# Performance work log

Measured on AMD Instinct MI355X. Metric: run time of the kernel, lower is better.

## Reference

```python
import jax, jax.numpy as jnp
import numpy as np
from jax import lax

INT8_NARROW = (-127.0, 127.0)   # brevitas Int8WeightPerTensorFloat (narrow range)
INT8_FULL = (-128.0, 127.0)     # brevitas Int8ActPerTensorFloat
INT32 = (-2.0**31, 2.0**31 - 1)


def _fake_quant(v, scale, qmin, qmax):
    # round-to-nearest, clip, dequant (per-tensor)
    return jnp.clip(jnp.round(v / scale), qmin, qmax) * scale


def _conv(x, w, stride):
    return lax.conv_general_dilated(
        x, w, window_strides=(stride, stride), padding=[(1, 1), (1, 1)],
        dimension_numbers=("NCHW", "OIHW", "NCHW"))


def setup_inputs() -> dict:
    key = jax.random.key(0)
    ks = jax.random.split(key, 5)
    B, Cin, Cout, H = 64, 256, 512, 28
    x = jax.random.normal(ks[0], (B, Cin, H, H), dtype=jnp.float32)
    w1 = jax.random.normal(ks[1], (Cout, Cin, 3, 3), dtype=jnp.float32) * 0.05
    b1 = jax.random.normal(ks[2], (Cout,), dtype=jnp.float32) * 0.01
    w2 = jax.random.normal(ks[3], (Cout, Cout, 3, 3), dtype=jnp.float32) * 0.05
    b2 = jax.random.normal(ks[4], (Cout,), dtype=jnp.float32) * 0.01
    return {
        "x": x, "w1": w1, "b1": b1, "w2": w2, "b2": b2,
        "in_scale": jnp.full((1,), 0.05, dtype=jnp.float32),
        "act1_scale": jnp.full((1,), 0.05, dtype=jnp.float32),
        "act2_scale": jnp.full((1,), 0.05, dtype=jnp.float32),
    }


def reference(x, w1, b1, w2, b2, in_scale, act1_scale, act2_scale):
    s_in = in_scale[0]
    s_a1 = act1_scale[0]
    s_a2 = act2_scale[0]

    # conv1: per-tensor int8 weight fake-quant (max-abs stats, narrow range)
    s_w1 = jnp.max(jnp.abs(w1)) / 127.0
    wq1 = _fake_quant(w1, s_w1, *INT8_NARROW)
    bq1 = _fake_quant(b1, s_in * s_w1, *INT32)  # Int32Bias: scale = in_scale*w_scale
    out = _conv(x, wq1, 2) + bq1[None, :, None, None]

    # act1: int8 activation fake-quant (learned per-tensor scale)
    out = _fake_quant(out, s_a1, *INT8_FULL)

    # conv2
    s_w2 = jnp.max(jnp.abs(w2)) / 127.0
    wq2 = _fake_quant(w2, s_w2, *INT8_NARROW)
    bq2 = _fake_quant(b2, s_a1 * s_w2, *INT32)
    out = _conv(out, wq2, 1) + bq2[None, :, None, None]

    # act2
    out = _fake_quant(out, s_a2, *INT8_FULL)
    return out
```

## Files before the change

kernel.cpp:

```cpp
#include <hip/hip_runtime.h>

typedef int i32x4 __attribute__((ext_vector_type(4)));

__device__ __forceinline__ void gl_lds16(const signed char* g, signed char* l) {
    __builtin_amdgcn_global_load_lds(
        (const __attribute__((address_space(1))) void*)g,
        (__attribute__((address_space(3))) void*)l, 16, 0, 0);
}

__device__ __forceinline__ unsigned lds_addr(const signed char* p) {
    return (unsigned)(uintptr_t)(const __attribute__((address_space(3))) signed char*)p;
}

__device__ __forceinline__ i32x4 lds_read_b128a(unsigned a) {
    i32x4 r;
    asm volatile("ds_read_b128 %0, %1" : "=v"(r) : "v"(a));
    return r;
}

#define XQ_SCALE 2048.0f
#define XQ_DELTA (1.0f / 2048.0f)

__device__ __forceinline__ float block_max256(const float* __restrict__ part, int base,
                                              float* __restrict__ sred) {
    float m = part[base + (threadIdx.x & 255)];
#pragma unroll
    for (int off = 32; off > 0; off >>= 1)
        m = fmaxf(m, __shfl_down(m, off));
    __syncthreads();
    if ((threadIdx.x & 63) == 0) sred[threadIdx.x >> 6] = m;
    __syncthreads();
    return fmaxf(fmaxf(sred[0], sred[1]), fmaxf(sred[2], sred[3]));
}

__global__ __launch_bounds__(256) void fused_pre_kernel(
    const float* __restrict__ x,
    const float* __restrict__ w1, const float* __restrict__ w2,
    float* __restrict__ part,
    signed char* __restrict__ xhi, signed char* __restrict__ xlo,
    signed char* __restrict__ act) {
    __shared__ float sred[4];
    const int blk = blockIdx.x;
    const int tid = threadIdx.x;
    const uint4 z = {0, 0, 0, 0};

    if (blk < 512) {
        const bool second = blk >= 256;
        const float* w = second ? w2 : w1;
        const int n4 = second ? 589824 : 294912;
        float m = 0.0f;
        for (int i = (blk & 255) * 256 + tid; i < n4; i += 65536) {
            float4 v = ((const float4*)w)[i];
            m = fmaxf(m, fmaxf(fmaxf(fabsf(v.x), fabsf(v.y)), fmaxf(fabsf(v.z), fabsf(v.w))));
        }
#pragma unroll
        for (int off = 32; off > 0; off >>= 1)
            m = fmaxf(m, __shfl_down(m, off));
        if ((tid & 63) == 0) sred[tid >> 6] = m;
        __syncthreads();
        if (tid == 0)
            part[blk] = fmaxf(fmaxf(sred[0], sred[1]), fmaxf(sred[2], sred[3]));
    } else if (blk < 976) {
        const int thr = (blk - 512) * 256 + tid;
        const int b = thr / (116 * 16);
        const int rr = thr - b * (116 * 16);
        const int p = rr >> 4;
        const int ch = rr & 15;
        int h, w;
        if (p < 30)      { h = 0;          w = p; }
        else if (p < 60) { h = 29;         w = p - 30; }
        else if (p < 88) { h = p - 60 + 1; w = 0; }
        else             { h = p - 88 + 1; w = 29; }
        const int off = (b * 900 + h * 30 + w) * 256 + ch * 16;
        *(uint4*)(xhi + off) = z;
        *(uint4*)(xlo + off) = z;
    } else if (blk < 1456) {
        const int thr = (blk - 976) * 256 + tid;
        const int b = thr / (60 * 32);
        const int rr = thr - b * (60 * 32);
        const int p = rr >> 5;
        const int ch = rr & 31;
        int h, w;
        if (p < 16)      { h = 0;          w = p; }
        else if (p < 32) { h = 15;         w = p - 16; }
        else if (p < 46) { h = p - 32 + 1; w = 0; }
        else             { h = p - 46 + 1; w = 15; }
        const int off = (b * 256 + h * 16 + w) * 512 + ch * 16;
        *(uint4*)(act + off) = z;
    } else {
        const int xb = blk - 1456;
        const int hwb = xb % 25;
        const int rest = xb / 25;
        const int cb = rest & 1;
        const int b = rest >> 1;
        const int c0 = cb * 128 + (tid >> 5) * 16;
        const int hw = hwb * 32 + (tid & 31);
        if (hw < 784) {
            const float* xp = x + (b * 256 + c0) * 784 + hw;
            union { signed char c[16]; uint4 u; } ph, pl;
#pragma unroll
            for (int j = 0; j < 16; ++j) {
                const float v = xp[j * 784];
                int q = (int)rintf(v * XQ_SCALE);
                q = max(-16383, min(16383, q));
                ph.c[j] = (signed char)(q >> 7);
                pl.c[j] = (signed char)(q & 127);
            }
            const int r = hw / 28;
            const int o = (b * 900 + (r + 1) * 30 + (hw - r * 28) + 1) * 256 + c0;
            *(uint4*)&xhi[o] = ph.u;
            *(uint4*)&xlo[o] = pl.u;
        }
    }
}

__global__ __launch_bounds__(256) void prep_w_kernel(
    const float* __restrict__ w1, const float* __restrict__ w2,
    const float* __restrict__ b1, const float* __restrict__ b2,
    const float* __restrict__ part,
    const float* __restrict__ in_scale, const float* __restrict__ act1_scale,
    signed char* __restrict__ wq1, signed char* __restrict__ wq2,
    float* __restrict__ bq1, float* __restrict__ bq2,
    float* __restrict__ wmax) {
    __shared__ __align__(16) signed char sw[4608];
    __shared__ float sred[4];
    const int blk = blockIdx.x;
    const int tid = threadIdx.x;

    if (blk < 512) {
        const float inv_s = 127.0f / block_max256(part, 0, sred);
        const int n = blk;
        const float4* src = (const float4*)(w1 + n * 2304);
#pragma unroll
        for (int rd = 0; rd < 3; ++rd) {
            const int f = rd * 256 + tid;
            if (f < 576) {
                const float4 v = src[f];
                float q0 = fminf(fmaxf(rintf(v.x * inv_s), -127.0f), 127.0f);
                float q1 = fminf(fmaxf(rintf(v.y * inv_s), -127.0f), 127.0f);
                float q2 = fminf(fmaxf(rintf(v.z * inv_s), -127.0f), 127.0f);
                float q3 = fminf(fmaxf(rintf(v.w * inv_s), -127.0f), 127.0f);
                const int i0 = f * 4;
                int cin, r;
                cin = i0 / 9;       r = i0 - cin * 9;       sw[r * 256 + cin] = (signed char)(int)q0;
                cin = (i0+1) / 9;   r = (i0+1) - cin * 9;   sw[r * 256 + cin] = (signed char)(int)q1;
                cin = (i0+2) / 9;   r = (i0+2) - cin * 9;   sw[r * 256 + cin] = (signed char)(int)q2;
                cin = (i0+3) / 9;   r = (i0+3) - cin * 9;   sw[r * 256 + cin] = (signed char)(int)q3;
            }
        }
        __syncthreads();
        if (tid < 144) *(uint4*)&wq1[n * 2304 + tid * 16] = *(const uint4*)&sw[tid * 16];
    } else if (blk < 1024) {
        const float inv_s = 127.0f / block_max256(part, 256, sred);
        const int n = blk - 512;
        const float4* src = (const float4*)(w2 + n * 4608);
#pragma unroll
        for (int rd = 0; rd < 5; ++rd) {
            const int f = rd * 256 + tid;
            if (f < 1152) {
                const float4 v = src[f];
                float q0 = fminf(fmaxf(rintf(v.x * inv_s), -127.0f), 127.0f);
                float q1 = fminf(fmaxf(rintf(v.y * inv_s), -127.0f), 127.0f);
                float q2 = fminf(fmaxf(rintf(v.z * inv_s), -127.0f), 127.0f);
                float q3 = fminf(fmaxf(rintf(v.w * inv_s), -127.0f), 127.0f);
                const int i0 = f * 4;
                int cin, r;
                cin = i0 / 9;       r = i0 - cin * 9;       sw[r * 512 + cin] = (signed char)(int)q0;
                cin = (i0+1) / 9;   r = (i0+1) - cin * 9;   sw[r * 512 + cin] = (signed char)(int)q1;
                cin = (i0+2) / 9;   r = (i0+2) - cin * 9;   sw[r * 512 + cin] = (signed char)(int)q2;
                cin = (i0+3) / 9;   r = (i0+3) - cin * 9;   sw[r * 512 + cin] = (signed char)(int)q3;
            }
        }
        __syncthreads();
        for (int o = tid; o < 288; o += 256)
            *(uint4*)&wq2[n * 4608 + o * 16] = *(const uint4*)&sw[o * 16];
    } else {
        const float m1 = block_max256(part, 0, sred);
        const float m2 = block_max256(part, 256, sred);
        if (tid == 0) { wmax[0] = m1; wmax[1] = m2; }
        for (int idx = tid; idx < 1024; idx += 256) {
            if (idx < 512) {
                const float s = (*in_scale) * (m1 * (1.0f / 127.0f));
                float q = rintf(b1[idx] / s);
                q = fminf(fmaxf(q, -2147483648.0f), 2147483648.0f);
                bq1[idx] = q * s;
            } else {
                const int j = idx - 512;
                const float s = (*act1_scale) * (m2 * (1.0f / 127.0f));
                float q = rintf(b2[j] / s);
                q = fminf(fmaxf(q, -2147483648.0f), 2147483648.0f);
                bq2[j] = q * s;
            }
        }
    }
}

template<int CIN, int STRIDE, int HP, int HOUT, bool SPLIT, bool FINAL>
__global__ __launch_bounds__(256, SPLIT ? 2 : 3) void conv_gemm_kernel(
    const signed char* __restrict__ Ahi,
    const signed char* __restrict__ Alo,
    const signed char* __restrict__ Wt,
    const float* __restrict__ bias,
    const float* __restrict__ wmax,
    const float* __restrict__ s_pre,
    const float* __restrict__ s_act,
    signed char* __restrict__ act_out,
    float* __restrict__ out_final)
{
    constexpr int K = 9 * CIN;
    constexpr int HW = HOUT * HOUT;
    constexpr int NIT = K / 128;
    constexpr int NC = SPLIT ? 8 : 6;
    constexpr int BUFSZ = SPLIT ? 32768 : 24576;
    constexpr int NB = SPLIT ? 4 : 2;

    __shared__ __align__(16) signed char smem[2 * BUFSZ];

    const int tid = threadIdx.x;
    const int lane = tid & 63;
    const int wv = tid >> 6;
    const int pair = wv >> 1;
    const int nh = wv & 1;
    const int quad = lane >> 4;
    const int l16 = lane & 15;

    const int lin = blockIdx.x + (int)gridDim.x * blockIdx.y;
    const int swz = (lin & 7) * 98 + (lin >> 3);
    const int n0 = (swz & 3) * 128;
    const int m0 = (swz >> 2) * 64;

    const int lrow = lane >> 3;
    const int koff = ((lane & 7) ^ lrow) * 16;

    const signed char* srcb[NC];
    int dsto[NC];
    bool isA[NC];
    if constexpr (SPLIT) {
#pragma unroll
        for (int i = 0; i < NC; ++i) {
            const int g = wv * 8 + i;
            const int type = g >> 3;
            if (type >= 2) {
                const int c = g - 16;
                srcb[i] = Wt + (n0 + c * 8 + lrow) * K + koff;
                dsto[i] = 16384 + c * 1024;
                isA[i] = false;
            } else {
                const int c = g & 7;
                const int m = m0 + c * 8 + lrow;
                const int b = m / HW;
                const int rem = m - b * HW;
                const int oh = rem / HOUT;
                const int ow = rem - oh * HOUT;
                const int off = ((b * HP + oh * STRIDE) * HP + ow * STRIDE) * CIN + koff;
                srcb[i] = (type == 0 ? Ahi : Alo) + off;
                dsto[i] = type * 8192 + c * 1024;
                isA[i] = true;
            }
        }
    } else {
#pragma unroll
        for (int i = 0; i < NC; ++i) {
            const int g = wv * 6 + i;
            if (g < 8) {
                const int c = g;
                const int m = m0 + c * 8 + lrow;
                const int b = m / HW;
                const int rem = m - b * HW;
                const int oh = rem / HOUT;
                const int ow = rem - oh * HOUT;
                const int off = ((b * HP + oh * STRIDE) * HP + ow * STRIDE) * CIN + koff;
                srcb[i] = Ahi + off;
                dsto[i] = c * 1024;
                isA[i] = true;
            } else {
                const int c = g - 8;
                srcb[i] = Wt + (n0 + c * 8 + lrow) * K + koff;
                dsto[i] = 8192 + c * 1024;
                isA[i] = false;
            }
        }
    }

    const int aoff0 = SPLIT ? (pair * 8192) : 0;
    const int boff0 = SPLIT ? 16384 : 8192;
    const int nfix  = SPLIT ? (nh * 64) : (wv * 32);

    unsigned aad[2][2][4];
    unsigned bad[2][2][NB];
#pragma unroll
    for (int bi = 0; bi < 2; ++bi)
#pragma unroll
        for (int ks = 0; ks < 2; ++ks) {
#pragma unroll
            for (int mi = 0; mi < 4; ++mi) {
                const int row = mi * 16 + l16;
                const int sl = ((ks * 4 + quad) ^ (row & 7)) * 16;
                aad[bi][ks][mi] = lds_addr(&smem[bi * BUFSZ + aoff0 + row * 128 + sl]);
            }
#pragma unroll
            for (int ni = 0; ni < NB; ++ni) {
                const int row = nfix + ni * 16 + l16;
                const int sl = ((ks * 4 + quad) ^ (row & 7)) * 16;
                bad[bi][ks][ni] = lds_addr(&smem[bi * BUFSZ + boff0 + row * 128 + sl]);
            }
        }

    i32x4 acc[4][NB];
#pragma unroll
    for (int mi = 0; mi < 4; ++mi)
#pragma unroll
        for (int ni = 0; ni < NB; ++ni)
            acc[mi][ni] = i32x4{0, 0, 0, 0};

    auto STAGE = [&](int bo, int it) {
        const int k0 = it * 128;
        const int r9 = k0 / CIN;
        const int kh = r9 / 3;
        const int kw = r9 - kh * 3;
        const int ashift = (kh * HP + kw) * CIN + (k0 & (CIN - 1));
#pragma unroll
        for (int i = 0; i < NC; ++i)
            gl_lds16(srcb[i] + (isA[i] ? ashift : k0), &smem[bo + dsto[i]]);
    };

    i32x4 af[2][4], bf[2][NB];

    auto LOADFRAGS = [&](int bi) {
#pragma unroll
        for (int ks = 0; ks < 2; ++ks) {
#pragma unroll
            for (int mi = 0; mi < 4; ++mi)
                af[ks][mi] = lds_read_b128a(aad[bi][ks][mi]);
#pragma unroll
            for (int ni = 0; ni < NB; ++ni)
                bf[ks][ni] = lds_read_b128a(bad[bi][ks][ni]);
        }
    };

    auto MFMAS_KS = [&](int ks) {
        __builtin_amdgcn_s_setprio(1);
#pragma unroll
        for (int mi = 0; mi < 4; ++mi)
#pragma unroll
            for (int ni = 0; ni < NB; ++ni)
                acc[mi][ni] = __builtin_amdgcn_mfma_i32_16x16x64_i8(af[ks][mi], bf[ks][ni], acc[mi][ni], 0, 0, 0);
        __builtin_amdgcn_s_setprio(0);
    };

    auto WAIT_NC = [&]() {
        if constexpr (SPLIT) asm volatile("s_waitcnt vmcnt(8)" ::: "memory");
        else                 asm volatile("s_waitcnt vmcnt(6)" ::: "memory");
    };
    auto LGKM_HALF = [&]() {
        if constexpr (SPLIT) asm volatile("s_waitcnt lgkmcnt(8)" ::: "memory");
        else                 asm volatile("s_waitcnt lgkmcnt(6)" ::: "memory");
    };

    STAGE(0, 0);
    STAGE(BUFSZ, 1);

    for (int it = 0; it < NIT - 2; it += 2) {
        WAIT_NC();
        __builtin_amdgcn_s_barrier();
        __builtin_amdgcn_sched_barrier(0);
        LOADFRAGS(0);
        LGKM_HALF();
        __builtin_amdgcn_sched_barrier(0);
        MFMAS_KS(0);
        asm volatile("s_waitcnt lgkmcnt(0)" ::: "memory");
        __builtin_amdgcn_sched_barrier(0);
        __builtin_amdgcn_s_barrier();
        __builtin_amdgcn_sched_barrier(0);
        STAGE(0, it + 2);
        MFMAS_KS(1);

        WAIT_NC();
        __builtin_amdgcn_s_barrier();
        __builtin_amdgcn_sched_barrier(0);
        LOADFRAGS(1);
        LGKM_HALF();
        __builtin_amdgcn_sched_barrier(0);
        MFMAS_KS(0);
        asm volatile("s_waitcnt lgkmcnt(0)" ::: "memory");
        __builtin_amdgcn_sched_barrier(0);
        __builtin_amdgcn_s_barrier();
        __builtin_amdgcn_sched_barrier(0);
        if (it + 3 < NIT) STAGE(BUFSZ, it + 3);
        MFMAS_KS(1);
    }

    WAIT_NC();
    __builtin_amdgcn_s_barrier();
    __builtin_amdgcn_sched_barrier(0);
    LOADFRAGS(0);
    LGKM_HALF();
    __builtin_amdgcn_sched_barrier(0);
    MFMAS_KS(0);
    asm volatile("s_waitcnt lgkmcnt(0)" ::: "memory");
    __builtin_amdgcn_sched_barrier(0);
    MFMAS_KS(1);

    asm volatile("s_waitcnt vmcnt(0)" ::: "memory");
    __builtin_amdgcn_s_barrier();
    __builtin_amdgcn_sched_barrier(0);
    LOADFRAGS(1);
    LGKM_HALF();
    __builtin_amdgcn_sched_barrier(0);
    MFMAS_KS(0);
    asm volatile("s_waitcnt lgkmcnt(0)" ::: "memory");
    __builtin_amdgcn_sched_barrier(0);
    MFMAS_KS(1);

    if constexpr (SPLIT) {
        __syncthreads();
        if (pair == 1) {
#pragma unroll
            for (int mi = 0; mi < 4; ++mi)
#pragma unroll
                for (int ni = 0; ni < 4; ++ni)
                    *(i32x4*)&smem[nh * 16384 + (mi * 4 + ni) * 1024 + lane * 16] = acc[mi][ni];
        }
        __syncthreads();
        if (pair == 1) return;
#pragma unroll
        for (int mi = 0; mi < 4; ++mi)
#pragma unroll
            for (int ni = 0; ni < 4; ++ni) {
                const i32x4 other = *(const i32x4*)&smem[nh * 16384 + (mi * 4 + ni) * 1024 + lane * 16];
                acc[mi][ni] = acc[mi][ni] * 128 + other;
            }
    }

    float alpha = (*wmax) * (1.0f / 127.0f);
    if (FINAL) alpha *= *s_pre;
    if (SPLIT) alpha *= XQ_DELTA;
    const float sact = *s_act;

    float bv[NB];
#pragma unroll
    for (int ni = 0; ni < NB; ++ni)
        bv[ni] = bias[n0 + nfix + ni * 16 + l16];

#pragma unroll
    for (int mi = 0; mi < 4; ++mi) {
#pragma unroll
        for (int i = 0; i < 4; ++i) {
            const int m = m0 + mi * 16 + quad * 4 + i;
            const int b = m / HW;
            const int rem = m - b * HW;
            const int oh = rem / HOUT;
            const int ow = rem - oh * HOUT;
#pragma unroll
            for (int ni = 0; ni < NB; ++ni) {
                const int col = n0 + nfix + ni * 16 + l16;
                const float v = (float)acc[mi][ni][i] * alpha + bv[ni];
                float q = rintf(v / sact);
                q = fminf(fmaxf(q, -128.0f), 127.0f);
                if (FINAL) {
                    out_final[(b * 512 + col) * HW + oh * HOUT + ow] = q * sact;
                } else {
                    act_out[(b * 256 + (oh + 1) * 16 + (ow + 1)) * 512 + col] = (signed char)(int)q;
                }
            }
        }
    }
}

extern "C" void kernel_launch(void* const* d_in, const int* in_sizes, int n_in,
                              void* d_out, int out_size, void* d_ws, size_t ws_size,
                              hipStream_t stream) {
    const float* x  = (const float*)d_in[0];
    const float* w1 = (const float*)d_in[1];
    const float* b1 = (const float*)d_in[2];
    const float* w2 = (const float*)d_in[3];
    const float* b2 = (const float*)d_in[4];
    const float* in_scale   = (const float*)d_in[5];
    const float* act1_scale = (const float*)d_in[6];
    const float* act2_scale = (const float*)d_in[7];
    float* out = (float*)d_out;

    char* ws = (char*)d_ws;
    float* part = (float*)(ws + 0);
    float* wmax = (float*)(ws + 2048);
    float* bq1 = (float*)(ws + 2176);
    float* bq2 = (float*)(ws + 4224);
    signed char* wq1 = (signed char*)(ws + 8192);
    signed char* wq2 = (signed char*)(ws + 1187840);
    signed char* xhi = (signed char*)(ws + 3547136);
    signed char* xlo = (signed char*)(ws + 18292736);
    signed char* act = (signed char*)(ws + 33038336);

    fused_pre_kernel<<<4656, 256, 0, stream>>>(x, w1, w2, part, xhi, xlo, act);

    prep_w_kernel<<<1025, 256, 0, stream>>>(w1, w2, b1, b2, part, in_scale, act1_scale,
                                            wq1, wq2, bq1, bq2, wmax);

    conv_gemm_kernel<256, 2, 30, 14, true, false><<<dim3(4, 196), 256, 0, stream>>>(
        xhi, xlo, wq1, bq1, wmax, act1_scale, act1_scale, act, nullptr);

    conv_gemm_kernel<512, 1, 16, 14, false, true><<<dim3(4, 196), 256, 0, stream>>>(
        act, nullptr, wq2, bq2, wmax + 1, act1_scale, act2_scale, nullptr, out);
}
```

Baseline: 221.3 us.

## Merge weight max-reduction and quantization into one kernel with grid-wide atomic barrier

Folds the per-tensor weight abs-max reduction and the weight/bias quantization into a single pre-processing kernel. Each of the first 1024 blocks reduces its own output channel, publishes the result via atomicMax plus a counter, then spin-waits until all 512 blocks of that tensor arrive before quantizing. A memset clears the counters. This removes one kernel launch and re-reads the weights while they are likely still cached, but relies on all 1024 spinning blocks being co-resident (launch bounds 8 per CU) to avoid deadlock, and adds spin-wait latency.

Result: slower. 346.3 us (+56.5%).

```diff
diff --git a/kernel.cpp b/kernel.cpp
--- a/kernel.cpp
+++ b/kernel.cpp
@@ -21,36 +21,33 @@
 #define XQ_SCALE 2048.0f
 #define XQ_DELTA (1.0f / 2048.0f)
 
-__device__ __forceinline__ float block_max256(const float* __restrict__ part, int base,
-                                              float* __restrict__ sred) {
-    float m = part[base + (threadIdx.x & 255)];
-#pragma unroll
-    for (int off = 32; off > 0; off >>= 1)
-        m = fmaxf(m, __shfl_down(m, off));
-    __syncthreads();
-    if ((threadIdx.x & 63) == 0) sred[threadIdx.x >> 6] = m;
-    __syncthreads();
-    return fmaxf(fmaxf(sred[0], sred[1]), fmaxf(sred[2], sred[3]));
-}
-
-__global__ __launch_bounds__(256) void fused_pre_kernel(
+__global__ __launch_bounds__(256, 8) void mega_pre_kernel(
     const float* __restrict__ x,
     const float* __restrict__ w1, const float* __restrict__ w2,
-    float* __restrict__ part,
+    const float* __restrict__ b1, const float* __restrict__ b2,
+    const float* __restrict__ in_scale, const float* __restrict__ act1_scale,
+    unsigned* __restrict__ syn,
+    float* __restrict__ wmax,
+    float* __restrict__ bq1, float* __restrict__ bq2,
+    signed char* __restrict__ wq1, signed char* __restrict__ wq2,
     signed char* __restrict__ xhi, signed char* __restrict__ xlo,
-    signed char* __restrict__ act) {
-    __shared__ float sred[4];
+    signed char* __restrict__ act)
+{
+    __shared__ __align__(16) signed char sw[4608];
+    __shared__ float sred[8];
     const int blk = blockIdx.x;
     const int tid = threadIdx.x;
     const uint4 z = {0, 0, 0, 0};
 
-    if (blk < 512) {
-        const bool second = blk >= 256;
-        const float* w = second ? w2 : w1;
-        const int n4 = second ? 589824 : 294912;
+    if (blk < 1024) {
+        const bool second = blk >= 512;
+        const int n = second ? (blk - 512) : blk;
+        const int NF = second ? 1152 : 576;
+        const float4* src = (const float4*)((second ? w2 : w1) + n * (NF * 4));
+
         float m = 0.0f;
-        for (int i = (blk & 255) * 256 + tid; i < n4; i += 65536) {
-            float4 v = ((const float4*)w)[i];
+        for (int f = tid; f < NF; f += 256) {
+            const float4 v = src[f];
             m = fmaxf(m, fmaxf(fmaxf(fabsf(v.x), fabsf(v.y)), fmaxf(fabsf(v.z), fabsf(v.w))));
         }
 #pragma unroll
@@ -58,10 +55,92 @@
             m = fmaxf(m, __shfl_down(m, off));
         if ((tid & 63) == 0) sred[tid >> 6] = m;
         __syncthreads();
-        if (tid == 0)
-            part[blk] = fmaxf(fmaxf(sred[0], sred[1]), fmaxf(sred[2], sred[3]));
-    } else if (blk < 976) {
-        const int thr = (blk - 512) * 256 + tid;
+        if (tid == 0) {
+            m = fmaxf(fmaxf(sred[0], sred[1]), fmaxf(sred[2], sred[3]));
+            const int ci = second ? 1 : 0;
+            atomicMax(&syn[2 + ci], __float_as_uint(m));
+            __hip_atomic_fetch_add(&syn[ci], 1u, __ATOMIC_RELEASE, __HIP_MEMORY_SCOPE_AGENT);
+            while (__hip_atomic_load(&syn[ci], __ATOMIC_ACQUIRE, __HIP_MEMORY_SCOPE_AGENT) < 512u)
+                __builtin_amdgcn_s_sleep(8);
+            sred[4] = __uint_as_float(
+                __hip_atomic_load(&syn[2 + ci], __ATOMIC_ACQUIRE, __HIP_MEMORY_SCOPE_AGENT));
+        }
+        __syncthreads();
+        const float inv_s = 127.0f / sred[4];
+
+        if (!second) {
+#pragma unroll
+            for (int rd = 0; rd < 3; ++rd) {
+                const int f = rd * 256 + tid;
+                if (f < 576) {
+                    const float4 v = src[f];
+                    float q0 = fminf(fmaxf(rintf(v.x * inv_s), -127.0f), 127.0f);
+                    float q1 = fminf(fmaxf(rintf(v.y * inv_s), -127.0f), 127.0f);
+                    float q2 = fminf(fmaxf(rintf(v.z * inv_s), -127.0f), 127.0f);
+                    float q3 = fminf(fmaxf(rintf(v.w * inv_s), -127.0f), 127.0f);
+                    const int i0 = f * 4;
+                    int cin, r;
+                    cin = i0 / 9;     r = i0 - cin * 9;     sw[r * 256 + cin] = (signed char)(int)q0;
+                    cin = (i0+1) / 9; r = (i0+1) - cin * 9; sw[r * 256 + cin] = (signed char)(int)q1;
+                    cin = (i0+2) / 9; r = (i0+2) - cin * 9; sw[r * 256 + cin] = (signed char)(int)q2;
+                    cin = (i0+3) / 9; r = (i0+3) - cin * 9; sw[r * 256 + cin] = (signed char)(int)q3;
+                }
+            }
+            __syncthreads();
+            if (tid < 144) *(uint4*)&wq1[n * 2304 + tid * 16] = *(const uint4*)&sw[tid * 16];
+        } else {
+#pragma unroll
+            for (int rd = 0; rd < 5; ++rd) {
+                const int f = rd * 256 + tid;
+                if (f < 1152) {
+                    const float4 v = src[f];
+                    float q0 = fminf(fmaxf(rintf(v.x * inv_s), -127.0f), 127.0f);
+                    float q1 = fminf(fmaxf(rintf(v.y * inv_s), -127.0f), 127.0f);
+                    float q2 = fminf(fmaxf(rintf(v.z * inv_s), -127.0f), 127.0f);
+                    float q3 = fminf(fmaxf(rintf(v.w * inv_s), -127.0f), 127.0f);
+                    const int i0 = f * 4;
+                    int cin, r;
+                    cin = i0 / 9;     r = i0 - cin * 9;     sw[r * 512 + cin] = (signed char)(int)q0;
+                    cin = (i0+1) / 9; r = (i0+1) - cin * 9; sw[r * 512 + cin] = (signed char)(int)q1;
+                    cin = (i0+2) / 9; r = (i0+2) - cin * 9; sw[r * 512 + cin] = (signed char)(int)q2;
+                    cin = (i0+3) / 9; r = (i0+3) - cin * 9; sw[r * 512 + cin] = (signed char)(int)q3;
+                }
+            }
+            __syncthreads();
+            for (int o = tid; o < 288; o += 256)
+                *(uint4*)&wq2[n * 4608 + o * 16] = *(const uint4*)&sw[o * 16];
+        }
+    } else if (blk == 1024) {
+        if (tid == 0) {
+            while (__hip_atomic_load(&syn[0], __ATOMIC_ACQUIRE, __HIP_MEMORY_SCOPE_AGENT) < 512u ||
+                   __hip_atomic_load(&syn[1], __ATOMIC_ACQUIRE, __HIP_MEMORY_SCOPE_AGENT) < 512u)
+                __builtin_amdgcn_s_sleep(8);
+            sred[4] = __uint_as_float(
+                __hip_atomic_load(&syn[2], __ATOMIC_ACQUIRE, __HIP_MEMORY_SCOPE_AGENT));
+            sred[5] = __uint_as_float(
+                __hip_atomic_load(&syn[3], __ATOMIC_ACQUIRE, __HIP_MEMORY_SCOPE_AGENT));
+            wmax[0] = sred[4];
+            wmax[1] = sred[5];
+        }
+        __syncthreads();
+        const float m1 = sred[4];
+        const float m2 = sred[5];
+        for (int idx = tid; idx < 1024; idx += 256) {
+            if (idx < 512) {
+                const float s = (*in_scale) * (m1 * (1.0f / 127.0f));
+                float q = rintf(b1[idx] / s);
+                q = fminf(fmaxf(q, -2147483648.0f), 2147483648.0f);
+                bq1[idx] = q * s;
+            } else {
+                const int j = idx - 512;
+                const float s = (*act1_scale) * (m2 * (1.0f / 127.0f));
+                float q = rintf(b2[j] / s);
+                q = fminf(fmaxf(q, -2147483648.0f), 2147483648.0f);
+                bq2[j] = q * s;
+            }
+        }
+    } else if (blk < 1489) {
+        const int thr = (blk - 1025) * 256 + tid;
         const int b = thr / (116 * 16);
         const int rr = thr - b * (116 * 16);
         const int p = rr >> 4;
@@ -74,8 +153,8 @@
         const int off = (b * 900 + h * 30 + w) * 256 + ch * 16;
         *(uint4*)(xhi + off) = z;
         *(uint4*)(xlo + off) = z;
-    } else if (blk < 1456) {
-        const int thr = (blk - 976) * 256 + tid;
+    } else if (blk < 1969) {
+        const int thr = (blk - 1489) * 256 + tid;
         const int b = thr / (60 * 32);
         const int rr = thr - b * (60 * 32);
         const int p = rr >> 5;
@@ -88,7 +167,7 @@
         const int off = (b * 256 + h * 16 + w) * 512 + ch * 16;
         *(uint4*)(act + off) = z;
     } else {
-        const int xb = blk - 1456;
+        const int xb = blk - 1969;
         const int hwb = xb % 25;
         const int rest = xb / 25;
         const int cb = rest & 1;
@@ -110,87 +189,6 @@
             const int o = (b * 900 + (r + 1) * 30 + (hw - r * 28) + 1) * 256 + c0;
             *(uint4*)&xhi[o] = ph.u;
             *(uint4*)&xlo[o] = pl.u;
-        }
-    }
-}
-
-__global__ __launch_bounds__(256) void prep_w_kernel(
-    const float* __restrict__ w1, const float* __restrict__ w2,
-    const float* __restrict__ b1, const float* __restrict__ b2,
-    const float* __restrict__ part,
-    const float* __restrict__ in_scale, const float* __restrict__ act1_scale,
-    signed char* __restrict__ wq1, signed char* __restrict__ wq2,
-    float* __restrict__ bq1, float* __restrict__ bq2,
-    float* __restrict__ wmax) {
-    __shared__ __align__(16) signed char sw[4608];
-    __shared__ float sred[4];
-    const int blk = blockIdx.x;
-    const int tid = threadIdx.x;
-
-    if (blk < 512) {
-        const float inv_s = 127.0f / block_max256(part, 0, sred);
-        const int n = blk;
-        const float4* src = (const float4*)(w1 + n * 2304);
-#pragma unroll
-        for (int rd = 0; rd < 3; ++rd) {
-            const int f = rd * 256 + tid;
-            if (f < 576) {
-                const float4 v = src[f];
-                float q0 = fminf(fmaxf(rintf(v.x * inv_s), -127.0f), 127.0f);
-                float q1 = fminf(fmaxf(rintf(v.y * inv_s), -127.0f), 127.0f);
-                float q2 = fminf(fmaxf(rintf(v.z * inv_s), -127.0f), 127.0f);
-                float q3 = fminf(fmaxf(rintf(v.w * inv_s), -127.0f), 127.0f);
-                const int i0 = f * 4;
-                int cin, r;
-                cin = i0 / 9;       r = i0 - cin * 9;       sw[r * 256 + cin] = (signed char)(int)q0;
-                cin = (i0+1) / 9;   r = (i0+1) - cin * 9;   sw[r * 256 + cin] = (signed char)(int)q1;
-                cin = (i0+2) / 9;   r = (i0+2) - cin * 9;   sw[r * 256 + cin] = (signed char)(int)q2;
-                cin = (i0+3) / 9;   r = (i0+3) - cin * 9;   sw[r * 256 + cin] = (signed char)(int)q3;
-            }
-        }
-        __syncthreads();
-        if (tid < 144) *(uint4*)&wq1[n * 2304 + tid * 16] = *(const uint4*)&sw[tid * 16];
-    } else if (blk < 1024) {
-        const float inv_s = 127.0f / block_max256(part, 256, sred);
-        const int n = blk - 512;
-        const float4* src = (const float4*)(w2 + n * 4608);
-#pragma unroll
-        for (int rd = 0; rd < 5; ++rd) {
-            const int f = rd * 256 + tid;
-            if (f < 1152) {
-                const float4 v = src[f];
-                float q0 = fminf(fmaxf(rintf(v.x * inv_s), -127.0f), 127.0f);
-                float q1 = fminf(fmaxf(rintf(v.y * inv_s), -127.0f), 127.0f);
-                float q2 = fminf(fmaxf(rintf(v.z * inv_s), -127.0f), 127.0f);
-                float q3 = fminf(fmaxf(rintf(v.w * inv_s), -127.0f), 127.0f);
-                const int i0 = f * 4;
-                int cin, r;
-                cin = i0 / 9;       r = i0 - cin * 9;       sw[r * 512 + cin] = (signed char)(int)q0;
-                cin = (i0+1) / 9;   r = (i0+1) - cin * 9;   sw[r * 512 + cin] = (signed char)(int)q1;
-                cin = (i0+2) / 9;   r = (i0+2) - cin * 9;   sw[r * 512 + cin] = (signed char)(int)q2;
-                cin = (i0+3) / 9;   r = (i0+3) - cin * 9;   sw[r * 512 + cin] = (signed char)(int)q3;
-            }
-        }
-        __syncthreads();
-        for (int o = tid; o < 288; o += 256)
-            *(uint4*)&wq2[n * 4608 + o * 16] = *(const uint4*)&sw[o * 16];
-    } else {
-        const float m1 = block_max256(part, 0, sred);
-        const float m2 = block_max256(part, 256, sred);
-        if (tid == 0) { wmax[0] = m1; wmax[1] = m2; }
-        for (int idx = tid; idx < 1024; idx += 256) {
-            if (idx < 512) {
-                const float s = (*in_scale) * (m1 * (1.0f / 127.0f));
-                float q = rintf(b1[idx] / s);
-                q = fminf(fmaxf(q, -2147483648.0f), 2147483648.0f);
-                bq1[idx] = q * s;
-            } else {
-                const int j = idx - 512;
-                const float s = (*act1_scale) * (m2 * (1.0f / 127.0f));
-                float q = rintf(b2[j] / s);
-                q = fminf(fmaxf(q, -2147483648.0f), 2147483648.0f);
-                bq2[j] = q * s;
-            }
         }
     }
 }
@@ -481,7 +479,7 @@
     float* out = (float*)d_out;
 
     char* ws = (char*)d_ws;
-    float* part = (float*)(ws + 0);
+    unsigned* syn = (unsigned*)(ws + 0);
     float* wmax = (float*)(ws + 2048);
     float* bq1 = (float*)(ws + 2176);
     float* bq2 = (float*)(ws + 4224);
@@ -491,10 +489,11 @@
     signed char* xlo = (signed char*)(ws + 18292736);
     signed char* act = (signed char*)(ws + 33038336);
 
-    fused_pre_kernel<<<4656, 256, 0, stream>>>(x, w1, w2, part, xhi, xlo, act);
-
-    prep_w_kernel<<<1025, 256, 0, stream>>>(w1, w2, b1, b2, part, in_scale, act1_scale,
-                                            wq1, wq2, bq1, bq2, wmax);
+    hipMemsetAsync(ws, 0, 16, stream);
+
+    mega_pre_kernel<<<5169, 256, 0, stream>>>(x, w1, w2, b1, b2, in_scale, act1_scale,
+                                              syn, wmax, bq1, bq2, wq1, wq2,
+                                              xhi, xlo, act);
 
     conv_gemm_kernel<256, 2, 30, 14, true, false><<<dim3(4, 196), 256, 0, stream>>>(
         xhi, xlo, wq1, bq1, wmax, act1_scale, act1_scale, act, nullptr);
```
